# Optimization experiments

Hardware: AMD Instinct MI355X
Metric: run time of the kernel (lower is better)

Reference implementation:

```python
import jax, jax.numpy as jnp
import numpy as np

N, E, B = 250000, 1000000, 500
FD = 78  # num_features_xd


def setup_inputs() -> dict:
    key = jax.random.key(0)
    ks = jax.random.split(key, 24)
    g = lambda i, shape, fan_in: jax.random.normal(ks[i], shape, jnp.float32) / np.sqrt(fan_in)
    inp = {
        "x": jax.random.normal(ks[0], (N, FD), jnp.float32),
        "edge_index": jax.random.randint(ks[1], (2, E), 0, N, jnp.int32),
        "batch": jnp.repeat(jnp.arange(B, dtype=jnp.int32), N // B),  # sorted, every graph non-empty
        "target": jax.random.randint(ks[2], (B, 1000), 0, 26, jnp.int32),
        # GCN layers
        "W1": g(3, (FD, FD), FD), "b1": jnp.zeros((FD,), jnp.float32),
        "W2": g(4, (FD, 2 * FD), FD), "b2": jnp.zeros((2 * FD,), jnp.float32),
        "W3": g(5, (2 * FD, 4 * FD), 2 * FD), "b3": jnp.zeros((4 * FD,), jnp.float32),
        # graph head
        "fcg1_w": g(6, (4 * FD, 1024), 4 * FD), "fcg1_b": jnp.zeros((1024,), jnp.float32),
        "fcg2_w": g(7, (1024, 128), 1024), "fcg2_b": jnp.zeros((128,), jnp.float32),
        # protein branch
        "emb": g(8, (26, 128), 1),
        "conv_w": g(9, (32, 1000, 8), 1000 * 8), "conv_b": jnp.zeros((32,), jnp.float32),
        "fcxt_w": g(10, (32 * 121, 128), 32 * 121), "fcxt_b": jnp.zeros((128,), jnp.float32),
        # fusion head
        "fc1_w": g(11, (256, 1024), 256), "fc1_b": jnp.zeros((1024,), jnp.float32),
        "fc2_w": g(12, (1024, 512), 1024), "fc2_b": jnp.zeros((512,), jnp.float32),
        "out_w": g(13, (512, 1), 512), "out_b": jnp.zeros((1,), jnp.float32),
    }
    return inp


def _gcn_conv(x, W, b, src, dst, dinv, n):
    # PyG GCNConv: out = D^-1/2 (A+I) D^-1/2 (x W) + b, symmetric norm with self-loops
    xw = x @ W
    norm = dinv[src] * dinv[dst]                                   # [E]
    agg = jax.ops.segment_sum(xw[src] * norm[:, None], dst, num_segments=n)
    agg = agg + xw * (dinv * dinv)[:, None]                        # self-loop term
    return agg + b


def reference(x, edge_index, batch, target,
              W1, b1, W2, b2, W3, b3,
              fcg1_w, fcg1_b, fcg2_w, fcg2_b,
              emb, conv_w, conv_b, fcxt_w, fcxt_b,
              fc1_w, fc1_b, fc2_w, fc2_b, out_w, out_b):
    n = x.shape[0]
    src, dst = edge_index[0], edge_index[1]
    # degree with self-loops (edge weights 1)
    deg = jax.ops.segment_sum(jnp.ones((src.shape[0],), x.dtype), dst, num_segments=n) + 1.0
    dinv = jax.lax.rsqrt(deg)

    h = jax.nn.relu(_gcn_conv(x, W1, b1, src, dst, dinv, n))
    h = jax.nn.relu(_gcn_conv(h, W2, b2, src, dst, dinv, n))
    h = jax.nn.relu(_gcn_conv(h, W3, b3, src, dst, dinv, n))

    bsz = fcg2_w.shape[1] * 0 + target.shape[0]  # B
    g = jax.ops.segment_max(h, batch, num_segments=bsz)            # global max pool -> [B, 312]
    g = jax.nn.relu(g @ fcg1_w + fcg1_b)
    g = g @ fcg2_w + fcg2_b                                        # dropout = identity (eval)

    # protein branch: Conv1d over embedding dim (channels = seq positions = 1000)
    e = emb[target]                                                # [B, 1000, 128]
    c = jax.lax.conv_general_dilated(e, conv_w, window_strides=(1,), padding="VALID",
                                     dimension_numbers=("NCH", "OIH", "NCH"))
    c = c + conv_b[None, :, None]                                  # [B, 32, 121]
    xt = c.reshape(bsz, 32 * 121) @ fcxt_w + fcxt_b

    xc = jnp.concatenate([g, xt], axis=1)                          # [B, 256]
    xc = jax.nn.relu(xc @ fc1_w + fc1_b)
    xc = jax.nn.relu(xc @ fc2_w + fc2_b)
    return xc @ out_w + out_b                                      # [B, 1]
```

## Files before the change

kernel.cpp:

```cpp
#include <hip/hip_runtime.h>
#include <hip/hip_bf16.h>

#define DEV_INLINE __device__ __forceinline__

static constexpr int Nn = 250000;
static constexpr int Ee = 1000000;
static constexpr int Bb = 500;
static constexpr int NPB = Nn / Bb;

typedef __attribute__((ext_vector_type(8))) short short8;
typedef __attribute__((ext_vector_type(8))) unsigned short ushort8v;
typedef __attribute__((ext_vector_type(4))) unsigned int uint4v;
typedef __attribute__((ext_vector_type(4))) float f32x4;
typedef __attribute__((ext_vector_type(2))) float f32x2;

DEV_INLINE float b2f(__hip_bfloat16 v) { return __bfloat162float(v); }
DEV_INLINE __hip_bfloat16 f2b(float v) { return __float2bfloat16(v); }
DEV_INLINE unsigned short f2bu(float v) {
    __hip_bfloat16 h = __float2bfloat16(v);
    return __builtin_bit_cast(unsigned short, h);
}
DEV_INLINE float bfu2f(unsigned short u) { return __uint_as_float(((unsigned)u) << 16); }

DEV_INLINE f32x2 pairf(unsigned u) {
    f32x2 r;
    r.x = __uint_as_float(u << 16);
    r.y = __uint_as_float(u & 0xffff0000u);
    return r;
}
DEV_INLINE f32x2 fma2(f32x2 a, f32x2 b, f32x2 c) {
#if __has_builtin(__builtin_elementwise_fma)
    return __builtin_elementwise_fma(a, b, c);
#else
    return a * b + c;
#endif
}

__global__ void k_deg(const int* __restrict__ dst, int* __restrict__ deg) {
    int i = blockIdx.x * 256 + threadIdx.x;
    if (i < Ee) atomicAdd(&deg[dst[i]], 1);
}

__global__ void k_dinv(const int* __restrict__ deg, float* __restrict__ dinv) {
    int i = blockIdx.x * 256 + threadIdx.x;
    if (i < Nn) dinv[i] = rsqrtf((float)deg[i] + 1.0f);
}

__global__ __launch_bounds__(256) void k_scan1(const int* __restrict__ deg,
                                               int* __restrict__ rp,
                                               int* __restrict__ bsum) {
    __shared__ int s[256];
    int t = threadIdx.x;
    int i = blockIdx.x * 256 + t;
    int v = (i < Nn) ? deg[i] : 0;
    s[t] = v;
    __syncthreads();
    for (int off = 1; off < 256; off <<= 1) {
        int x = (t >= off) ? s[t - off] : 0;
        __syncthreads();
        s[t] += x;
        __syncthreads();
    }
    if (i < Nn) rp[i] = s[t] - v;
    if (t == 255) bsum[blockIdx.x] = s[255];
}

__global__ __launch_bounds__(1024) void k_scan2(int* __restrict__ bsum, int nb) {
    __shared__ int s[1024];
    int t = threadIdx.x;
    int v = (t < nb) ? bsum[t] : 0;
    s[t] = v;
    __syncthreads();
    for (int off = 1; off < 1024; off <<= 1) {
        int x = (t >= off) ? s[t - off] : 0;
        __syncthreads();
        s[t] += x;
        __syncthreads();
    }
    if (t < nb) bsum[t] = s[t] - v;
}

__global__ void k_scan3(int* __restrict__ rp, int* __restrict__ cursor,
                        const int* __restrict__ bsum) {
    int i = blockIdx.x * 256 + threadIdx.x;
    if (i < Nn) {
        int v = rp[i] + bsum[blockIdx.x];
        rp[i] = v;
        cursor[i] = v;
    }
    if (i == 0) rp[Nn] = Ee;
}

__global__ void k_scatter(const int* __restrict__ src, const int* __restrict__ dst,
                          const float* __restrict__ dinv, int* __restrict__ cursor,
                          int* __restrict__ col, float* __restrict__ enorm) {
    int i = blockIdx.x * 256 + threadIdx.x;
    if (i >= Ee) return;
    int s = src[i], d = dst[i];
    int pos = atomicAdd(&cursor[d], 1);
    col[pos] = s;
    enorm[pos] = dinv[s] * dinv[d];
}

__global__ void k_xprep(const float* __restrict__ x, unsigned short* __restrict__ xb) {
    int gid = blockIdx.x * 256 + threadIdx.x;
    if (gid >= Nn * 20) return;
    int i = gid / 20;
    int c = gid - 20 * i;
    int k = 4 * c;
    const float* xp = x + (size_t)i * 78;
    ushort4 u;
    u.x = (k + 0 < 78) ? f2bu(xp[k + 0]) : (unsigned short)0;
    u.y = (k + 1 < 78) ? f2bu(xp[k + 1]) : (unsigned short)0;
    u.z = (k + 2 < 78) ? f2bu(xp[k + 2]) : (unsigned short)0;
    u.w = (k + 3 < 78) ? f2bu(xp[k + 3]) : (unsigned short)0;
    *(ushort4*)&xb[(size_t)i * 80 + k] = u;
}

template <int K, int F, int KP, int FP>
__global__ __launch_bounds__(64) void k_wprep(const float* __restrict__ W,
                                              unsigned short* __restrict__ Wb) {
    constexpr int KSTEPS = KP / 32;
    const int nt = blockIdx.x, ks = blockIdx.y;
    const int l = threadIdx.x;
    const int n = nt * 16 + (l & 15);
    unsigned short* o = Wb + ((size_t)(nt * KSTEPS + ks) * 64 + l) * 8;
#pragma unroll
    for (int j = 0; j < 8; ++j) {
        const int k = (l >> 4) * 8 + j + ks * 32;
        o[j] = (k < K && n < F) ? f2bu(W[(size_t)k * F + n]) : (unsigned short)0;
    }
}

template <int KIN, int KP, int F, int FP, int SOUT, bool POOL, int MAXROWS>
__global__ __launch_bounds__(320, 8) void k_gcn(const __hip_bfloat16* __restrict__ in_,
                                                const int* __restrict__ rp,
                                                const int* __restrict__ col,
                                                const float* __restrict__ enorm,
                                                const float* __restrict__ dinv,
                                                const unsigned short* __restrict__ Wb,
                                                const float* __restrict__ bias,
                                                __hip_bfloat16* __restrict__ out,
                                                float* __restrict__ gpool) {
    constexpr int BD = 320, WAVES = 5;
    constexpr int CPR = KIN / 8;
    constexpr int ECAP = 16 * MAXROWS;
    constexpr int KSTEPS = KP / 32;
    constexpr int NT = FP / 16;
    constexpr int TPW = NT / WAVES;
    static_assert(KIN % 8 == 0 && KP % 32 == 0 && KP >= KIN && FP % (16 * WAVES) == 0, "pad");
    static_assert(MAXROWS % 16 == 0, "row tiles");
    static_assert(!POOL || MAXROWS == 16, "pool path assumes 16 rows");
    static_assert(CPR * MAXROWS == BD, "one slot per thread");
    const unsigned short* in = (const unsigned short*)in_;

    __shared__ alignas(16) unsigned short sh[MAXROWS * KP];
    __shared__ int sRp[MAXROWS + 1];
    __shared__ int sCol[ECAP];
    __shared__ float sEn[ECAP];

    const int i0 = blockIdx.x * MAXROWS;
    const int rows = min(MAXROWS, Nn - i0);
    const int t = threadIdx.x;
    const int slots = rows * CPR;
    const bool act = (t < slots);

    const int r = t / CPR;
    const int c = t - r * CPR;
    const size_t coff = (size_t)8 * c;
    uint4v selfv = {0u, 0u, 0u, 0u};
    float selfw = 0.f;
    if (act) {
        const int i = i0 + r;
        selfv = *(const uint4v*)(in + (size_t)i * KIN + coff);
        const float di = dinv[i];
        selfw = di * di;
    }

    if (t <= rows) sRp[t] = rp[i0 + t];
    const int base = rp[i0];
    const int ne = rp[i0 + rows] - base;
    const bool fit = (ne <= ECAP);
    if (fit) {
        for (int e = t; e < ne; e += BD) {
            sCol[e] = col[base + e];
            sEn[e] = enorm[base + e];
        }
    }
    if constexpr (KP > KIN) {
        for (int e = t; e < MAXROWS * (KP - KIN); e += BD) {
            const int rr = e / (KP - KIN);
            sh[rr * KP + KIN + (e - rr * (KP - KIN))] = 0;
        }
    }
    __syncthreads();

    if (act) {
        f32x2 acc2[4];
#pragma unroll
        for (int q = 0; q < 4; ++q) acc2[q] = pairf(selfv[q]) * selfw;

        const int e0a = sRp[r], e1a = sRp[r + 1];
        if (fit) {
            int j = e0a - base;
            const int jend = e1a - base;
            for (; j + 4 <= jend; j += 4) {
                const int n0 = sCol[j + 0], n1 = sCol[j + 1], n2 = sCol[j + 2], n3 = sCol[j + 3];
                const float w0 = sEn[j + 0], w1 = sEn[j + 1], w2 = sEn[j + 2], w3 = sEn[j + 3];
                uint4v a0 = *(const uint4v*)(in + (size_t)n0 * KIN + coff);
                uint4v a1 = *(const uint4v*)(in + (size_t)n1 * KIN + coff);
                uint4v a2 = *(const uint4v*)(in + (size_t)n2 * KIN + coff);
                uint4v a3 = *(const uint4v*)(in + (size_t)n3 * KIN + coff);
                const f32x2 w0v = {w0, w0}, w1v = {w1, w1}, w2v = {w2, w2}, w3v = {w3, w3};
#pragma unroll
                for (int q = 0; q < 4; ++q) {
                    acc2[q] = fma2(pairf(a0[q]), w0v, acc2[q]);
                    acc2[q] = fma2(pairf(a1[q]), w1v, acc2[q]);
                    acc2[q] = fma2(pairf(a2[q]), w2v, acc2[q]);
                    acc2[q] = fma2(pairf(a3[q]), w3v, acc2[q]);
                }
            }
            for (; j < jend; ++j) {
                const int n = sCol[j];
                const float wv = sEn[j];
                const f32x2 wvv = {wv, wv};
                uint4v a = *(const uint4v*)(in + (size_t)n * KIN + coff);
#pragma unroll
                for (int q = 0; q < 4; ++q) acc2[q] = fma2(pairf(a[q]), wvv, acc2[q]);
            }
        } else {
            for (int j = e0a; j < e1a; ++j) {
                const int n = col[j];
                const float wv = enorm[j];
                const f32x2 wvv = {wv, wv};
                uint4v a = *(const uint4v*)(in + (size_t)n * KIN + coff);
#pragma unroll
                for (int q = 0; q < 4; ++q) acc2[q] = fma2(pairf(a[q]), wvv, acc2[q]);
            }
        }
        ushort8v o;
#pragma unroll
        for (int q = 0; q < 4; ++q) {
            o[2 * q + 0] = f2bu(acc2[q].x);
            o[2 * q + 1] = f2bu(acc2[q].y);
        }
        *(ushort8v*)&sh[r * KP + 8 * c] = o;
    }
    __syncthreads();

    const int w = t >> 6, lane = t & 63;
    const int arow = lane & 15, aquad = lane >> 4;
    const int nrt = rows >> 4;

    for (int rt = 0; rt < nrt; ++rt) {
        short8 afr[KSTEPS];
#pragma unroll
        for (int ks = 0; ks < KSTEPS; ++ks)
            afr[ks] = *(const short8*)&sh[(rt * 16 + arow) * KP + aquad * 8 + ks * 32];

        const int ir0 = i0 + rt * 16;
        const bool uni = (ir0 / NPB) == ((ir0 + 15) / NPB);

#pragma unroll
        for (int nti = 0; nti < TPW; ++nti) {
            const int nt = w * TPW + nti;
            const short8* bp = (const short8*)Wb + (size_t)nt * KSTEPS * 64 + lane;
            f32x4 acc = {0.f, 0.f, 0.f, 0.f};
#pragma unroll
            for (int ks = 0; ks < KSTEPS; ++ks) {
                short8 bfr = bp[ks * 64];
                acc = __builtin_amdgcn_mfma_f32_16x16x32_bf16(afr[ks], bfr, acc, 0, 0, 0);
            }
            const int f = nt * 16 + arow;
            const int ib = ir0 + aquad * 4;
            if constexpr (!POOL) {
                if (f < F) {
                    const float bv = bias[f];
#pragma unroll
                    for (int rr = 0; rr < 4; ++rr)
                        out[(size_t)(ib + rr) * SOUT + f] = f2b(fmaxf(acc[rr] + bv, 0.f));
                } else if (f < SOUT) {
#pragma unroll
                    for (int rr = 0; rr < 4; ++rr)
                        out[(size_t)(ib + rr) * SOUT + f] = f2b(0.f);
                }
            } else {
                float m = 0.f, v[4];
                const float bv = (f < F) ? bias[f] : 0.f;
#pragma unroll
                for (int rr = 0; rr < 4; ++rr) {
                    v[rr] = fmaxf(acc[rr] + bv, 0.f);
                    m = fmaxf(m, v[rr]);
                }
                if (uni) {
                    m = fmaxf(m, __shfl_xor(m, 16));
                    m = fmaxf(m, __shfl_xor(m, 32));
                    if (aquad == 0 && f < F)
                        atomicMax((int*)&gpool[(ir0 / NPB) * F + f], __float_as_int(m));
                } else if (f < F) {
                    const int g0 = ib / NPB, g3 = (ib + 3) / NPB;
                    if (g0 == g3) {
                        atomicMax((int*)&gpool[g0 * F + f], __float_as_int(m));
                    } else {
#pragma unroll
                        for (int rr = 0; rr < 4; ++rr)
                            atomicMax((int*)&gpool[((ib + rr) / NPB) * F + f], __float_as_int(v[rr]));
                    }
                }
            }
        }
    }
}

template <int K, int FOUT, int KS, bool RELU, int BD>
__global__ __launch_bounds__(BD) void k_fc(const float* __restrict__ in,
                                           const float* __restrict__ W,
                                           const float* __restrict__ bias,
                                           float* __restrict__ out,
                                           int ostride, int ooff) {
    static_assert(!(RELU && KS > 1), "cannot split K with fused ReLU");
    static_assert(K % KS == 0, "K must divide evenly");
    constexpr int KC = K / KS;
    const int j = blockIdx.x * BD + threadIdx.x;
    const int b = blockIdx.y;
    const int z = blockIdx.z;
    const float* __restrict__ inp = in + (size_t)b * K + z * KC;
    const float* __restrict__ Wp = W + (size_t)(z * KC) * FOUT + j;
    float acc = (z == 0) ? bias[j] : 0.f;
#pragma unroll 8
    for (int k = 0; k < KC; ++k) acc += inp[k] * Wp[(size_t)k * FOUT];
    float* dst = &out[(size_t)b * ostride + ooff + j];
    if (KS > 1) {
        atomicAdd(dst, acc);
    } else {
        *dst = RELU ? fmaxf(acc, 0.f) : acc;
    }
}

__global__ __launch_bounds__(128) void k_P(const float* __restrict__ emb,
                                           const float* __restrict__ fcxt_w,
                                           float* __restrict__ P) {
    const int v = blockIdx.x, o = blockIdx.y;
    const int j = threadIdx.x;
    __shared__ float se[128];
    se[j] = emb[v * 128 + j];
    __syncthreads();
    float acc[8];
#pragma unroll
    for (int k = 0; k < 8; ++k) acc[k] = 0.f;
    const float* fw = fcxt_w + (size_t)(o * 121) * 128 + j;
#pragma unroll 4
    for (int h = 0; h < 121; ++h) {
        const float f = fw[(size_t)h * 128];
#pragma unroll
        for (int k = 0; k < 8; ++k) acc[k] += se[h + k] * f;
    }
    float* Pp = P + ((size_t)(v * 32 + o) * 8) * 128 + j;
#pragma unroll
    for (int k = 0; k < 8; ++k) Pp[(size_t)k * 128] = acc[k];
}

__global__ __launch_bounds__(128) void k_T(const float* __restrict__ convw,
                                           const float* __restrict__ P,
                                           float* __restrict__ T) {
    const int i0 = blockIdx.x * 8;
    const int v = blockIdx.y;
    const int t = threadIdx.x;
    __shared__ float wt[8 * 256];
    for (int e = t; e < 2048; e += 128) {
        const int r = e >> 8;
        const int kk = e & 255;
        wt[e] = convw[(size_t)(kk >> 3) * 8000 + (size_t)(i0 + r) * 8 + (kk & 7)];
    }
    __syncthreads();
    float acc[8];
#pragma unroll
    for (int r = 0; r < 8; ++r) acc[r] = 0.f;
    const float* Pp = P + (size_t)v * 256 * 128 + t;
#pragma unroll 2
    for (int kk = 0; kk < 256; ++kk) {
        const float pv = Pp[(size_t)kk * 128];
#pragma unroll
        for (int r = 0; r < 8; ++r) acc[r] += wt[r * 256 + kk] * pv;
    }
    float* Tp = T + ((size_t)v * 1000 + i0) * 128 + t;
#pragma unroll
    for (int r = 0; r < 8; ++r) Tp[(size_t)r * 128] = acc[r];
}

__global__ __launch_bounds__(128) void k_C0(const float* __restrict__ fcxt_w,
                                            const float* __restrict__ fcxt_b,
                                            const float* __restrict__ convb,
                                            float* __restrict__ C0) {
    const int o = blockIdx.x;
    const int j = threadIdx.x;
    float acc = 0.f;
    const float* fw = fcxt_w + (size_t)(o * 121) * 128 + j;
#pragma unroll 4
    for (int h = 0; h < 121; ++h) acc += fw[(size_t)h * 128];
    acc *= convb[o];
    if (o == 0) acc += fcxt_b[j];
    atomicAdd(&C0[j], acc);
}

template <int ZS>
__global__ __launch_bounds__(128) void k_xt(const int* __restrict__ target,
                                            const float* __restrict__ T,
                                            const float* __restrict__ C0,
                                            float* __restrict__ xc) {
    constexpr int CH = 1000 / ZS;
    const int b = blockIdx.x;
    const int z = blockIdx.y;
    const int j = threadIdx.x;
    const int* tg = target + b * 1000 + z * CH;
    float acc = (z == 0) ? C0[j] : 0.f;
    int i = 0;
    for (; i + 4 <= CH; i += 4) {
        const int v0 = tg[i + 0], v1 = tg[i + 1], v2 = tg[i + 2], v3 = tg[i + 3];
        const int ib = z * CH + i;
        acc += T[((size_t)v0 * 1000 + ib + 0) * 128 + j]
             + T[((size_t)v1 * 1000 + ib + 1) * 128 + j]
             + T[((size_t)v2 * 1000 + ib + 2) * 128 + j]
             + T[((size_t)v3 * 1000 + ib + 3) * 128 + j];
    }
    for (; i < CH; ++i) {
        acc += T[((size_t)tg[i] * 1000 + z * CH + i) * 128 + j];
    }
    atomicAdd(&xc[(size_t)b * 256 + 128 + j], acc);
}

__global__ __launch_bounds__(64) void k_out(const float* __restrict__ in,
                                            const float* __restrict__ w,
                                            const float* __restrict__ ob,
                                            float* __restrict__ out) {
    const int b = blockIdx.x;
    const int lane = threadIdx.x;
    const float* p = in + (size_t)b * 512;
    float acc = 0.f;
#pragma unroll
    for (int i = 0; i < 8; ++i) acc += p[lane + 64 * i] * w[lane + 64 * i];
    for (int off = 32; off > 0; off >>= 1) acc += __shfl_down(acc, off);
    if (lane == 0) out[b] = acc + ob[0];
}

extern "C" void kernel_launch(void* const* d_in, const int* in_sizes, int n_in,
                              void* d_out, int out_size, void* d_ws, size_t ws_size,
                              hipStream_t stream) {
    (void)in_sizes; (void)n_in; (void)out_size; (void)ws_size;
    const float* x      = (const float*)d_in[0];
    const int* ei       = (const int*)d_in[1];
    const int* target   = (const int*)d_in[3];
    const float* W1     = (const float*)d_in[4];
    const float* b1     = (const float*)d_in[5];
    const float* W2     = (const float*)d_in[6];
    const float* b2     = (const float*)d_in[7];
    const float* W3     = (const float*)d_in[8];
    const float* b3     = (const float*)d_in[9];
    const float* fcg1_w = (const float*)d_in[10];
    const float* fcg1_b = (const float*)d_in[11];
    const float* fcg2_w = (const float*)d_in[12];
    const float* fcg2_b = (const float*)d_in[13];
    const float* emb    = (const float*)d_in[14];
    const float* conv_w = (const float*)d_in[15];
    const float* conv_b = (const float*)d_in[16];
    const float* fcxt_w = (const float*)d_in[17];
    const float* fcxt_b = (const float*)d_in[18];
    const float* fc1_w  = (const float*)d_in[19];
    const float* fc1_b  = (const float*)d_in[20];
    const float* fc2_w  = (const float*)d_in[21];
    const float* fc2_b  = (const float*)d_in[22];
    const float* out_w  = (const float*)d_in[23];
    const float* out_b  = (const float*)d_in[24];

    const int* src = ei;
    const int* dst = ei + Ee;

    size_t off = 0;
    auto alloc = [&](size_t bytes) -> void* {
        off = (off + 255) & ~(size_t)255;
        void* p = (char*)d_ws + off;
        off += bytes;
        return p;
    };
    int*   deg    = (int*)alloc((size_t)Nn * 4);
    float* dinv   = (float*)alloc((size_t)Nn * 4);
    int*   rp     = (int*)alloc((size_t)(Nn + 1) * 4);
    int*   col    = (int*)alloc((size_t)Ee * 4);
    float* enorm  = (float*)alloc((size_t)Ee * 4);
    int*   bsum   = (int*)alloc(1024 * 4);
    unsigned short* Wb1 = (unsigned short*)alloc((size_t)5 * 3 * 64 * 8 * 2);
    unsigned short* Wb2 = (unsigned short*)alloc((size_t)10 * 3 * 64 * 8 * 2);
    unsigned short* Wb3 = (unsigned short*)alloc((size_t)20 * 5 * 64 * 8 * 2);
    __hip_bfloat16* h1 = (__hip_bfloat16*)alloc((size_t)Nn * 80 * 2);
    __hip_bfloat16* h2 = (__hip_bfloat16*)alloc((size_t)Nn * 160 * 2);
    int* cursor = deg;
    unsigned short* xb = (unsigned short*)h2;

    size_t hoff = 0;
    auto halloc = [&](size_t bytes) -> void* {
        hoff = (hoff + 255) & ~(size_t)255;
        void* p = (char*)h1 + hoff;
        hoff += bytes;
        return p;
    };
    float* gpool = (float*)halloc((size_t)Bb * 312 * 4);
    float* g1    = (float*)halloc((size_t)Bb * 1024 * 4);
    float* xc    = (float*)halloc((size_t)Bb * 256 * 4);
    float* f1    = (float*)halloc((size_t)Bb * 1024 * 4);
    float* f2    = (float*)halloc((size_t)Bb * 512 * 4);
    float* C0    = (float*)halloc(128 * 4);
    float* Pbuf  = (float*)halloc((size_t)26 * 32 * 8 * 128 * 4);
    float* Tbuf  = (float*)halloc((size_t)26 * 1000 * 128 * 4);

    const int nb = (Nn + 255) / 256;

    k_xprep<<<(Nn * 20 + 255) / 256, 256, 0, stream>>>(x, xb);

    hipMemsetAsync(deg, 0, (size_t)Nn * 4, stream);
    k_deg<<<(Ee + 255) / 256, 256, 0, stream>>>(dst, deg);
    k_dinv<<<nb, 256, 0, stream>>>(deg, dinv);
    k_scan1<<<nb, 256, 0, stream>>>(deg, rp, bsum);
    k_scan2<<<1, 1024, 0, stream>>>(bsum, nb);
    k_scan3<<<nb, 256, 0, stream>>>(rp, cursor, bsum);
    k_scatter<<<(Ee + 255) / 256, 256, 0, stream>>>(src, dst, dinv, cursor, col, enorm);

    k_wprep<78, 78, 96, 80><<<dim3(5, 3), 64, 0, stream>>>(W1, Wb1);
    k_wprep<78, 156, 96, 160><<<dim3(10, 3), 64, 0, stream>>>(W2, Wb2);
    k_wprep<156, 312, 160, 320><<<dim3(20, 5), 64, 0, stream>>>(W3, Wb3);

    const int g32 = (Nn + 31) / 32;
    k_gcn<80, 96, 78, 80, 80, false, 32><<<g32, 320, 0, stream>>>(
        (const __hip_bfloat16*)xb, rp, col, enorm, dinv, Wb1, b1, h1, (float*)nullptr);
    k_gcn<80, 96, 156, 160, 160, false, 32><<<g32, 320, 0, stream>>>(
        h1, rp, col, enorm, dinv, Wb2, b2, h2, (float*)nullptr);
    hipMemsetAsync(gpool, 0, (size_t)Bb * 312 * 4, stream);
    k_gcn<160, 160, 312, 320, 0, true, 16><<<Nn / 16, 320, 0, stream>>>(
        h2, rp, col, enorm, dinv, Wb3, b3, (__hip_bfloat16*)nullptr, gpool);

    hipMemsetAsync(C0, 0, 128 * 4, stream);
    hipMemsetAsync(xc, 0, (size_t)Bb * 256 * 4, stream);
    k_P<<<dim3(26, 32), 128, 0, stream>>>(emb, fcxt_w, Pbuf);
    k_T<<<dim3(125, 26), 128, 0, stream>>>(conv_w, Pbuf, Tbuf);
    k_C0<<<32, 128, 0, stream>>>(fcxt_w, fcxt_b, conv_b, C0);
    k_xt<8><<<dim3(Bb, 8), 128, 0, stream>>>(target, Tbuf, C0, xc);

    k_fc<312, 1024, 1, true, 256><<<dim3(4, Bb, 1), 256, 0, stream>>>(gpool, fcg1_w, fcg1_b, g1, 1024, 0);
    k_fc<1024, 128, 2, false, 128><<<dim3(1, Bb, 2), 128, 0, stream>>>(g1, fcg2_w, fcg2_b, xc, 256, 0);

    k_fc<256, 1024, 1, true, 256><<<dim3(4, Bb, 1), 256, 0, stream>>>(xc, fc1_w, fc1_b, f1, 1024, 0);
    k_fc<1024, 512, 1, true, 256><<<dim3(2, Bb, 1), 256, 0, stream>>>(f1, fc2_w, fc2_b, f2, 512, 0);
    k_out<<<Bb, 64, 0, stream>>>(f2, out_w, out_b, (float*)d_out);
}
```

Baseline: 844.2 us.

## Aggregate GCN neighbours with MFMA over a block-local sparse weight matrix

The neighbour aggregation no longer uses per-thread FMA gathers. Each 16-row block gathers up to 96 neighbour and self rows cooperatively into LDS in MFMA B-fragment layout, builds a bf16 one-hot-weighted A matrix, and reduces with 16x16x32 bf16 MFMAs. All layers now use 16-row blocks at lower occupancy. The goal is fully coalesced, parallel gathers and less VALU work. The cost is more LDS, extra syncs, padded wasted MFMA work, and bf16 rounding of edge norms. Blocks with too many edges fall back to the scalar path.

```diff
diff --git a/kernel.cpp b/kernel.cpp
--- a/kernel.cpp
+++ b/kernel.cpp
@@ -14,13 +14,11 @@
 typedef __attribute__((ext_vector_type(4))) float f32x4;
 typedef __attribute__((ext_vector_type(2))) float f32x2;
 
-DEV_INLINE float b2f(__hip_bfloat16 v) { return __bfloat162float(v); }
 DEV_INLINE __hip_bfloat16 f2b(float v) { return __float2bfloat16(v); }
 DEV_INLINE unsigned short f2bu(float v) {
     __hip_bfloat16 h = __float2bfloat16(v);
     return __builtin_bit_cast(unsigned short, h);
 }
-DEV_INLINE float bfu2f(unsigned short u) { return __uint_as_float(((unsigned)u) << 16); }
 
 DEV_INLINE f32x2 pairf(unsigned u) {
     f32x2 r;
@@ -132,8 +130,8 @@
     }
 }
 
-template <int KIN, int KP, int F, int FP, int SOUT, bool POOL, int MAXROWS>
-__global__ __launch_bounds__(320, 8) void k_gcn(const __hip_bfloat16* __restrict__ in_,
+template <int KIN, int KP, int F, int FP, int SOUT, bool POOL>
+__global__ __launch_bounds__(320, 4) void k_gcn(const __hip_bfloat16* __restrict__ in_,
                                                 const int* __restrict__ rp,
                                                 const int* __restrict__ col,
                                                 const float* __restrict__ enorm,
@@ -142,170 +140,206 @@
                                                 const float* __restrict__ bias,
                                                 __hip_bfloat16* __restrict__ out,
                                                 float* __restrict__ gpool) {
-    constexpr int BD = 320, WAVES = 5;
+    constexpr int BD = 320, WAVES = 5, ROWS = 16;
     constexpr int CPR = KIN / 8;
-    constexpr int ECAP = 16 * MAXROWS;
+    constexpr int EK = 96, EKS = EK / 32;
+    constexpr int EMAX = EK - ROWS;
+    constexpr int NTIN = KIN / 16;
+    constexpr int ATPW = NTIN / WAVES;
+    constexpr int NCH = EK * CPR / BD;
     constexpr int KSTEPS = KP / 32;
     constexpr int NT = FP / 16;
     constexpr int TPW = NT / WAVES;
-    static_assert(KIN % 8 == 0 && KP % 32 == 0 && KP >= KIN && FP % (16 * WAVES) == 0, "pad");
-    static_assert(MAXROWS % 16 == 0, "row tiles");
-    static_assert(!POOL || MAXROWS == 16, "pool path assumes 16 rows");
-    static_assert(CPR * MAXROWS == BD, "one slot per thread");
+    constexpr int FRS = 64 * 8 + 16;
+    static_assert(KIN % 16 == 0 && KP % 32 == 0 && KP >= KIN, "pad");
+    static_assert(FP % (16 * WAVES) == 0 && NTIN % WAVES == 0, "waves");
+    static_assert(EK * CPR % BD == 0, "chunks");
     const unsigned short* in = (const unsigned short*)in_;
 
-    __shared__ alignas(16) unsigned short sh[MAXROWS * KP];
-    __shared__ int sRp[MAXROWS + 1];
-    __shared__ int sCol[ECAP];
-    __shared__ float sEn[ECAP];
-
-    const int i0 = blockIdx.x * MAXROWS;
-    const int rows = min(MAXROWS, Nn - i0);
+    __shared__ alignas(16) unsigned short sNbr[NTIN * EKS * FRS];
+    __shared__ alignas(16) unsigned short aWgt[EKS * 64 * 8];
+    __shared__ alignas(16) unsigned short sh[ROWS * KP];
+    __shared__ int sRp[ROWS + 1];
+    __shared__ unsigned char sRowX[EK];
+    __shared__ unsigned short sEnB[EK];
+
+    const int i0 = blockIdx.x * ROWS;
     const int t = threadIdx.x;
-    const int slots = rows * CPR;
-    const bool act = (t < slots);
-
-    const int r = t / CPR;
-    const int c = t - r * CPR;
-    const size_t coff = (size_t)8 * c;
-    uint4v selfv = {0u, 0u, 0u, 0u};
-    float selfw = 0.f;
-    if (act) {
-        const int i = i0 + r;
-        selfv = *(const uint4v*)(in + (size_t)i * KIN + coff);
-        const float di = dinv[i];
-        selfw = di * di;
-    }
-
-    if (t <= rows) sRp[t] = rp[i0 + t];
+
+    if (t <= ROWS) sRp[t] = rp[i0 + t];
     const int base = rp[i0];
-    const int ne = rp[i0 + rows] - base;
-    const bool fit = (ne <= ECAP);
+    const int ne = rp[i0 + ROWS] - base;
+    const int netot = ne + ROWS;
+    const bool fit = (ne <= EMAX);
+
+    if constexpr (KP > KIN) {
+        if (t < ROWS * (KP - KIN)) {
+            const int r = t / (KP - KIN);
+            sh[r * KP + KIN + (t - r * (KP - KIN))] = 0;
+        }
+    }
+
     if (fit) {
-        for (int e = t; e < ne; e += BD) {
-            sCol[e] = col[base + e];
-            sEn[e] = enorm[base + e];
-        }
-    }
-    if constexpr (KP > KIN) {
-        for (int e = t; e < MAXROWS * (KP - KIN); e += BD) {
-            const int rr = e / (KP - KIN);
-            sh[rr * KP + KIN + (e - rr * (KP - KIN))] = 0;
-        }
-    }
-    __syncthreads();
-
-    if (act) {
-        f32x2 acc2[4];
-#pragma unroll
-        for (int q = 0; q < 4; ++q) acc2[q] = pairf(selfv[q]) * selfw;
-
-        const int e0a = sRp[r], e1a = sRp[r + 1];
-        if (fit) {
-            int j = e0a - base;
-            const int jend = e1a - base;
-            for (; j + 4 <= jend; j += 4) {
-                const int n0 = sCol[j + 0], n1 = sCol[j + 1], n2 = sCol[j + 2], n3 = sCol[j + 3];
-                const float w0 = sEn[j + 0], w1 = sEn[j + 1], w2 = sEn[j + 2], w3 = sEn[j + 3];
-                uint4v a0 = *(const uint4v*)(in + (size_t)n0 * KIN + coff);
-                uint4v a1 = *(const uint4v*)(in + (size_t)n1 * KIN + coff);
-                uint4v a2 = *(const uint4v*)(in + (size_t)n2 * KIN + coff);
-                uint4v a3 = *(const uint4v*)(in + (size_t)n3 * KIN + coff);
-                const f32x2 w0v = {w0, w0}, w1v = {w1, w1}, w2v = {w2, w2}, w3v = {w3, w3};
-#pragma unroll
-                for (int q = 0; q < 4; ++q) {
-                    acc2[q] = fma2(pairf(a0[q]), w0v, acc2[q]);
-                    acc2[q] = fma2(pairf(a1[q]), w1v, acc2[q]);
-                    acc2[q] = fma2(pairf(a2[q]), w2v, acc2[q]);
-                    acc2[q] = fma2(pairf(a3[q]), w3v, acc2[q]);
+        if (t < ne) sEnB[t] = f2bu(enorm[base + t]);
+        if (t < ROWS) {
+            const int ea = rp[i0 + t] - base, eb = rp[i0 + t + 1] - base;
+            for (int j2 = ea; j2 < eb; ++j2) sRowX[j2] = (unsigned char)t;
+        } else if (t < 2 * ROWS) {
+            const int r = t - ROWS;
+            const float d = dinv[i0 + r];
+            sRowX[ne + r] = (unsigned char)r;
+            sEnB[ne + r] = f2bu(d * d);
+        } else if (t - 2 * ROWS < EK - netot) {
+            sRowX[netot + (t - 2 * ROWS)] = 255;
+        }
+        uint4v vch[NCH];
+#pragma unroll
+        for (int kk = 0; kk < NCH; ++kk) {
+            const int ch = kk * BD + t;
+            const int e = ch / CPR, c = ch - e * CPR;
+            int n;
+            if (e < ne) n = col[base + e];
+            else if (e < netot) n = i0 + (e - ne);
+            else n = i0;
+            vch[kk] = *(const uint4v*)(in + (size_t)n * KIN + (size_t)8 * c);
+        }
+        __syncthreads();
+#pragma unroll
+        for (int kk = 0; kk < NCH; ++kk) {
+            const int ch = kk * BD + t;
+            const int e = ch / CPR, c = ch - e * CPR;
+            const int eks = e >> 5, q32 = e & 31, quad = q32 >> 3, j = q32 & 7;
+            const int nt_in = c >> 1, colb = (c & 1) * 8;
+            unsigned short* p = &sNbr[(nt_in * EKS + eks) * FRS + (quad * 16 + colb) * 8 + j];
+#pragma unroll
+            for (int q = 0; q < 8; ++q) {
+                const unsigned u = vch[kk][q >> 1];
+                p[q * 8] = (unsigned short)((q & 1) ? (u >> 16) : (u & 0xffffu));
+            }
+        }
+        if (t < EKS * 64) {
+            const int l = t & 63;
+            const int m = l & 15, quad = l >> 4;
+            const int e0 = (t >> 6) * 32 + quad * 8;
+            ushort8v o;
+#pragma unroll
+            for (int j = 0; j < 8; ++j) {
+                const int e = e0 + j;
+                o[j] = (sRowX[e] == (unsigned char)m) ? sEnB[e] : (unsigned short)0;
+            }
+            *(ushort8v*)&aWgt[(size_t)t * 8] = o;
+        }
+        __syncthreads();
+        {
+            const int wv = t >> 6, lane = t & 63;
+            f32x4 agga[ATPW];
+#pragma unroll
+            for (int tl = 0; tl < ATPW; ++tl) agga[tl] = f32x4{0.f, 0.f, 0.f, 0.f};
+#pragma unroll
+            for (int eks = 0; eks < EKS; ++eks) {
+                short8 afrg = *(const short8*)&aWgt[(eks * 64 + lane) * 8];
+#pragma unroll
+                for (int tl = 0; tl < ATPW; ++tl) {
+                    const int nt_in = wv * ATPW + tl;
+                    short8 bfrg = *(const short8*)&sNbr[(nt_in * EKS + eks) * FRS + lane * 8];
+                    agga[tl] = __builtin_amdgcn_mfma_f32_16x16x32_bf16(afrg, bfrg, agga[tl], 0, 0, 0);
                 }
             }
-            for (; j < jend; ++j) {
-                const int n = sCol[j];
-                const float wv = sEn[j];
-                const f32x2 wvv = {wv, wv};
+#pragma unroll
+            for (int tl = 0; tl < ATPW; ++tl) {
+                const int nt_in = wv * ATPW + tl;
+                const int cc = nt_in * 16 + (lane & 15);
+                const int r0 = (lane >> 4) * 4;
+#pragma unroll
+                for (int reg = 0; reg < 4; ++reg)
+                    sh[(r0 + reg) * KP + cc] = f2bu(agga[tl][reg]);
+            }
+        }
+    } else {
+        __syncthreads();
+        const int slots = ROWS * CPR;
+        if (t < slots) {
+            const int r = t / CPR, c = t - r * CPR;
+            const size_t coff = (size_t)8 * c;
+            const int i = i0 + r;
+            const float di = dinv[i];
+            const float selfw = di * di;
+            f32x2 acc2[4];
+            uint4v sv = *(const uint4v*)(in + (size_t)i * KIN + coff);
+#pragma unroll
+            for (int q = 0; q < 4; ++q) acc2[q] = pairf(sv[q]) * selfw;
+            for (int j2 = sRp[r]; j2 < sRp[r + 1]; ++j2) {
+                const int n = col[j2];
+                const float wv2 = enorm[j2];
+                const f32x2 wvv = {wv2, wv2};
                 uint4v a = *(const uint4v*)(in + (size_t)n * KIN + coff);
 #pragma unroll
                 for (int q = 0; q < 4; ++q) acc2[q] = fma2(pairf(a[q]), wvv, acc2[q]);
             }
-        } else {
-            for (int j = e0a; j < e1a; ++j) {
-                const int n = col[j];
-                const float wv = enorm[j];
-                const f32x2 wvv = {wv, wv};
-                uint4v a = *(const uint4v*)(in + (size_t)n * KIN + coff);
-#pragma unroll
-                for (int q = 0; q < 4; ++q) acc2[q] = fma2(pairf(a[q]), wvv, acc2[q]);
-            }
-        }
-        ushort8v o;
-#pragma unroll
-        for (int q = 0; q < 4; ++q) {
-            o[2 * q + 0] = f2bu(acc2[q].x);
-            o[2 * q + 1] = f2bu(acc2[q].y);
-        }
-        *(ushort8v*)&sh[r * KP + 8 * c] = o;
+            ushort8v o;
+#pragma unroll
+            for (int q = 0; q < 4; ++q) {
+                o[2 * q + 0] = f2bu(acc2[q].x);
+                o[2 * q + 1] = f2bu(acc2[q].y);
+            }
+            *(ushort8v*)&sh[r * KP + 8 * c] = o;
+        }
     }
     __syncthreads();
 
     const int w = t >> 6, lane = t & 63;
     const int arow = lane & 15, aquad = lane >> 4;
-    const int nrt = rows >> 4;
-
-    for (int rt = 0; rt < nrt; ++rt) {
-        short8 afr[KSTEPS];
-#pragma unroll
-        for (int ks = 0; ks < KSTEPS; ++ks)
-            afr[ks] = *(const short8*)&sh[(rt * 16 + arow) * KP + aquad * 8 + ks * 32];
-
-        const int ir0 = i0 + rt * 16;
-        const bool uni = (ir0 / NPB) == ((ir0 + 15) / NPB);
-
-#pragma unroll
-        for (int nti = 0; nti < TPW; ++nti) {
-            const int nt = w * TPW + nti;
-            const short8* bp = (const short8*)Wb + (size_t)nt * KSTEPS * 64 + lane;
-            f32x4 acc = {0.f, 0.f, 0.f, 0.f};
-#pragma unroll
-            for (int ks = 0; ks < KSTEPS; ++ks) {
-                short8 bfr = bp[ks * 64];
-                acc = __builtin_amdgcn_mfma_f32_16x16x32_bf16(afr[ks], bfr, acc, 0, 0, 0);
-            }
-            const int f = nt * 16 + arow;
-            const int ib = ir0 + aquad * 4;
-            if constexpr (!POOL) {
-                if (f < F) {
-                    const float bv = bias[f];
+    short8 afr[KSTEPS];
+#pragma unroll
+    for (int ks = 0; ks < KSTEPS; ++ks)
+        afr[ks] = *(const short8*)&sh[arow * KP + aquad * 8 + ks * 32];
+
+    const bool uni = (i0 / NPB) == ((i0 + ROWS - 1) / NPB);
+
+#pragma unroll
+    for (int nti = 0; nti < TPW; ++nti) {
+        const int nt = w * TPW + nti;
+        const short8* bp = (const short8*)Wb + (size_t)nt * KSTEPS * 64 + lane;
+        f32x4 acc = {0.f, 0.f, 0.f, 0.f};
+#pragma unroll
+        for (int ks = 0; ks < KSTEPS; ++ks) {
+            short8 bfr = bp[ks * 64];
+            acc = __builtin_amdgcn_mfma_f32_16x16x32_bf16(afr[ks], bfr, acc, 0, 0, 0);
+        }
+        const int f = nt * 16 + arow;
+        const int ib = i0 + aquad * 4;
+        if constexpr (!POOL) {
+            if (f < F) {
+                const float bv = bias[f];
+#pragma unroll
+                for (int rr = 0; rr < 4; ++rr)
+                    out[(size_t)(ib + rr) * SOUT + f] = f2b(fmaxf(acc[rr] + bv, 0.f));
+            } else if (f < SOUT) {
+#pragma unroll
+                for (int rr = 0; rr < 4; ++rr)
+                    out[(size_t)(ib + rr) * SOUT + f] = f2b(0.f);
+            }
+        } else {
+            float m = 0.f, v[4];
+            const float bv = (f < F) ? bias[f] : 0.f;
+#pragma unroll
+            for (int rr = 0; rr < 4; ++rr) {
+                v[rr] = fmaxf(acc[rr] + bv, 0.f);
+                m = fmaxf(m, v[rr]);
+            }
+            if (uni) {
+                m = fmaxf(m, __shfl_xor(m, 16));
+                m = fmaxf(m, __shfl_xor(m, 32));
+                if (aquad == 0 && f < F)
+                    atomicMax((int*)&gpool[(i0 / NPB) * F + f], __float_as_int(m));
+            } else if (f < F) {
+                const int g0 = ib / NPB, g3 = (ib + 3) / NPB;
+                if (g0 == g3) {
+                    atomicMax((int*)&gpool[g0 * F + f], __float_as_int(m));
+                } else {
 #pragma unroll
                     for (int rr = 0; rr < 4; ++rr)
-                        out[(size_t)(ib + rr) * SOUT + f] = f2b(fmaxf(acc[rr] + bv, 0.f));
-                } else if (f < SOUT) {
-#pragma unroll
-                    for (int rr = 0; rr < 4; ++rr)
-                        out[(size_t)(ib + rr) * SOUT + f] = f2b(0.f);
-                }
-            } else {
-                float m = 0.f, v[4];
-                const float bv = (f < F) ? bias[f] : 0.f;
-#pragma unroll
-                for (int rr = 0; rr < 4; ++rr) {
-                    v[rr] = fmaxf(acc[rr] + bv, 0.f);
-                    m = fmaxf(m, v[rr]);
-                }
-                if (uni) {
-                    m = fmaxf(m, __shfl_xor(m, 16));
-                    m = fmaxf(m, __shfl_xor(m, 32));
-                    if (aquad == 0 && f < F)
-                        atomicMax((int*)&gpool[(ir0 / NPB) * F + f], __float_as_int(m));
-                } else if (f < F) {
-                    const int g0 = ib / NPB, g3 = (ib + 3) / NPB;
-                    if (g0 == g3) {
-                        atomicMax((int*)&gpool[g0 * F + f], __float_as_int(m));
-                    } else {
-#pragma unroll
-                        for (int rr = 0; rr < 4; ++rr)
-                            atomicMax((int*)&gpool[((ib + rr) / NPB) * F + f], __float_as_int(v[rr]));
-                    }
+                        atomicMax((int*)&gpool[((ib + rr) / NPB) * F + f], __float_as_int(v[rr]));
                 }
             }
         }
@@ -528,13 +562,13 @@
     k_wprep<78, 156, 96, 160><<<dim3(10, 3), 64, 0, stream>>>(W2, Wb2);
     k_wprep<156, 312, 160, 320><<<dim3(20, 5), 64, 0, stream>>>(W3, Wb3);
 
-    const int g32 = (Nn + 31) / 32;
-    k_gcn<80, 96, 78, 80, 80, false, 32><<<g32, 320, 0, stream>>>(
+    const int gg = Nn / 16;
+    k_gcn<80, 96, 78, 80, 80, false><<<gg, 320, 0, stream>>>(
         (const __hip_bfloat16*)xb, rp, col, enorm, dinv, Wb1, b1, h1, (float*)nullptr);
-    k_gcn<80, 96, 156, 160, 160, false, 32><<<g32, 320, 0, stream>>>(
+    k_gcn<80, 96, 156, 160, 160, false><<<gg, 320, 0, stream>>>(
         h1, rp, col, enorm, dinv, Wb2, b2, h2, (float*)nullptr);
     hipMemsetAsync(gpool, 0, (size_t)Bb * 312 * 4, stream);
-    k_gcn<160, 160, 312, 320, 0, true, 16><<<Nn / 16, 320, 0, stream>>>(
+    k_gcn<160, 160, 312, 320, 0, true><<<gg, 320, 0, stream>>>(
         h2, rp, col, enorm, dinv, Wb3, b3, (__hip_bfloat16*)nullptr, gpool);
 
     hipMemsetAsync(C0, 0, 128 * 4, stream);
```

Measured after the change: 1.011 ms. 19.8% more time.
